# Performance work log

Hardware: AMD Instinct MI355X
Metric: run time of the kernel (lower is better)

Reference implementation:

```python
import jax, jax.numpy as jnp
import numpy as np

B = 16384       # batch
NCAT = 16       # number of categorical features / tokens
VOCAB = 1000    # per-feature vocab size
D = 64          # embedding_dim / d_model
H = 4           # num_heads
SHARED = 10     # max(1, int(64 * 1/6))
INDIV = D - SHARED  # 54
CONT = 16       # continuous feature dim
L = 2           # layers per encoder
FLAT = NCAT * D + CONT  # 1040, MLP input dim
EPS = 1e-5


def _ln(x, w, b):
    m = x.mean(-1, keepdims=True)
    v = ((x - m) ** 2).mean(-1, keepdims=True)
    return (x - m) / jnp.sqrt(v + EPS) * w + b


def _encoder(x, qkv_w, out_w, ln1w, ln1b, ln2w, ln2b, w1, b1, w2, b2):
    # x: [b, t, d]; stacked per-layer params have leading dim L, scanned over.
    b, t, d = x.shape
    dh = d // H
    scale = dh ** -0.5

    def step(carry, p):
        x, prev = carry
        qw, ow, l1w, l1b, l2w, l2b, fw1, fb1, fw2, fb2 = p
        xn = _ln(x, l1w, l1b)
        qkv = xn @ qw                       # [b, t, 3d]
        q, k, v = jnp.split(qkv, 3, axis=-1)
        q = q.reshape(b, t, H, dh).transpose(0, 2, 1, 3)  # [b, h, t, dh]
        k = k.reshape(b, t, H, dh).transpose(0, 2, 1, 3)
        v = v.reshape(b, t, H, dh).transpose(0, 2, 1, 3)
        scores = jnp.einsum('bhid,bhjd->bhij', q, k) * scale + prev
        attn = jax.nn.softmax(scores, axis=-1)
        o = jnp.einsum('bhij,bhjd->bhid', attn, v)
        o = o.transpose(0, 2, 1, 3).reshape(b, t, d) @ ow
        x = x + o
        ff = jax.nn.gelu(_ln(x, l2w, l2b) @ fw1 + fb1, approximate=False) @ fw2 + fb2
        # prev_attn is detached in the torch code
        return (x + ff, jax.lax.stop_gradient(scores)), None

    prev0 = jnp.zeros((b, H, t, t), x.dtype)
    (x, _), _ = jax.lax.scan(step, (x, prev0),
                             (qkv_w, out_w, ln1w, ln1b, ln2w, ln2b, w1, b1, w2, b2))
    return x


def setup_inputs() -> dict:
    key = jax.random.key(0)
    ks = iter(jax.random.split(key, 64))

    def rn(shape, s=0.02):
        return jax.random.normal(next(ks), shape, jnp.float32) * s

    inp = {}
    inp['x_cat'] = jax.random.randint(next(ks), (B, NCAT), 0, VOCAB)
    inp['x_cont'] = jax.random.normal(next(ks), (B, CONT), jnp.float32)
    inp['shared_emb'] = rn((SHARED,), 1.0)
    inp['emb_tables'] = rn((NCAT, VOCAB, INDIV), 1.0)
    for pfx in ('mi', 'ma'):
        inp[pfx + '_qkv'] = rn((L, D, 3 * D))
        inp[pfx + '_out'] = rn((L, D, D))
        inp[pfx + '_ln1w'] = jnp.ones((L, D)); inp[pfx + '_ln1b'] = jnp.zeros((L, D))
        inp[pfx + '_ln2w'] = jnp.ones((L, D)); inp[pfx + '_ln2b'] = jnp.zeros((L, D))
        inp[pfx + '_w1'] = rn((L, D, 4 * D)); inp[pfx + '_b1'] = jnp.zeros((L, 4 * D))
        inp[pfx + '_w2'] = rn((L, 4 * D, D)); inp[pfx + '_b2'] = jnp.zeros((L, D))
    inp['cont_w'] = rn((CONT, CONT)); inp['cont_b'] = jnp.zeros((CONT,))
    inp['mlp_w1'] = rn((FLAT, 4 * FLAT)); inp['mlp_b1'] = jnp.zeros((4 * FLAT,))
    inp['mlp_w2'] = rn((4 * FLAT, 2 * FLAT)); inp['mlp_b2'] = jnp.zeros((2 * FLAT,))
    inp['mlp_w3'] = rn((2 * FLAT, 1)); inp['mlp_b3'] = jnp.zeros((1,))
    return inp


def reference(x_cat, x_cont, shared_emb, emb_tables,
              mi_qkv, mi_out, mi_ln1w, mi_ln1b, mi_ln2w, mi_ln2b, mi_w1, mi_b1, mi_w2, mi_b2,
              ma_qkv, ma_out, ma_ln1w, ma_ln1b, ma_ln2w, ma_ln2b, ma_w1, ma_b1, ma_w2, ma_b2,
              cont_w, cont_b, mlp_w1, mlp_b1, mlp_w2, mlp_b2, mlp_w3, mlp_b3):
    b = x_cat.shape[0]
    # embed: shared prefix + per-feature individual embedding -> [b, NCAT, D]
    indiv = emb_tables[jnp.arange(NCAT)[None, :], x_cat]          # [b, NCAT, INDIV]
    shared = jnp.broadcast_to(shared_emb, (b, NCAT, SHARED))
    tokens = jnp.concatenate([shared, indiv], axis=-1)
    # micro encoder on tokens (0, 1)
    micro = _encoder(tokens[:, :2, :], mi_qkv, mi_out, mi_ln1w, mi_ln1b,
                     mi_ln2w, mi_ln2b, mi_w1, mi_b1, mi_w2, mi_b2)
    tokens = tokens.at[:, :2, :].set(micro)
    # macro encoder on all tokens
    macro = _encoder(tokens, ma_qkv, ma_out, ma_ln1w, ma_ln1b,
                     ma_ln2w, ma_ln2b, ma_w1, ma_b1, ma_w2, ma_b2)
    flat = macro.reshape(b, NCAT * D)
    cont = x_cont @ cont_w + cont_b
    x = jnp.concatenate([flat, cont], axis=-1)
    h = jax.nn.gelu(x @ mlp_w1 + mlp_b1, approximate=False)
    h = jax.nn.gelu(h @ mlp_w2 + mlp_b2, approximate=False)
    logits = (h @ mlp_w3 + mlp_b3)[:, 0]
    return logits
```

## Files before the change

### kernel.cpp

```cpp
#include <hip/hip_runtime.h>
#include <hip/hip_bf16.h>
#include <math.h>

#define BATCH  16384
#define NCATS  16
#define VOCABN 1000
#define DIMD   64
#define SHARED_E 10
#define INDIVE 54
#define CONTN  16
#define FLATN  1040
#define H1N    4160
#define H2N    2080
#define KP1    1088
#define NP1    4224
#define KP2    4224
#define NP2    2176
#define EPSV   1e-5f

typedef __attribute__((ext_vector_type(8))) short bf16x8;
typedef __attribute__((ext_vector_type(4))) float f32x4;

__device__ __forceinline__ float gelu_f(float x) {
    return 0.5f * x * (1.0f + erff(x * 0.70710678118654752440f));
}
__device__ __forceinline__ float wsum(float v) {
#pragma unroll
    for (int o = 32; o > 0; o >>= 1) v += __shfl_xor(v, o, 64);
    return v;
}
__device__ __forceinline__ short f2bf_s(float a) {
    __hip_bfloat16 x = __float2bfloat16(a);
    return *reinterpret_cast<short*>(&x);
}
__device__ __forceinline__ unsigned int packbf(float a, float b) {
    __hip_bfloat16 x = __float2bfloat16(a), y = __float2bfloat16(b);
    unsigned short ux = *reinterpret_cast<unsigned short*>(&x);
    unsigned short uy = *reinterpret_cast<unsigned short*>(&y);
    return (unsigned)ux | ((unsigned)uy << 16);
}
__device__ __forceinline__ float bf_lo(unsigned int u) { return __uint_as_float(u << 16); }
__device__ __forceinline__ float bf_hi(unsigned int u) { return __uint_as_float(u & 0xffff0000u); }
__device__ __forceinline__ void gload16(const void* g, void* l) {
    __builtin_amdgcn_global_load_lds(
        (const __attribute__((address_space(1))) void*)g,
        (__attribute__((address_space(3))) void*)l, 16, 0, 0);
}

__global__ __launch_bounds__(256) void build_tokens(
    const int* __restrict__ x_cat, const float* __restrict__ shared_emb,
    const float* __restrict__ emb, float* __restrict__ xflat)
{
    int idx = blockIdx.x * 256 + threadIdx.x;
    int b = idx >> 10, r = idx & 1023;
    int c = r >> 6, d = r & 63;
    float v;
    if (d < SHARED_E) v = shared_emb[d];
    else              v = emb[((size_t)c * VOCABN + x_cat[b * NCATS + c]) * INDIVE + (d - SHARED_E)];
    xflat[(size_t)b * FLATN + r] = v;
}

__global__ __launch_bounds__(256) void cont_proj(
    const float* __restrict__ x_cont, const float* __restrict__ cw,
    const float* __restrict__ cb, float* __restrict__ xflat)
{
    int idx = blockIdx.x * 256 + threadIdx.x;
    int b = idx >> 4, j = idx & 15;
    float acc = cb[j];
#pragma unroll
    for (int k = 0; k < 16; ++k) acc += x_cont[b * 16 + k] * cw[k * 16 + j];
    xflat[(size_t)b * FLATN + 1024 + j] = acc;
}

__global__ __launch_bounds__(64) void micro_enc_mfma(
    float* __restrict__ xflat, const short* __restrict__ wT,
    const float* __restrict__ ln1w, const float* __restrict__ ln1b,
    const float* __restrict__ ln2w, const float* __restrict__ ln2b,
    const float* __restrict__ b1, const float* __restrict__ b2)
{
    __shared__ __align__(16) float Xr[16][68];
    __shared__ __align__(16) short XN[16][72];
    __shared__ __align__(16) short KVb[16][136];
    __shared__ __align__(16) short Qb[16][72];

    int lane = threadIdx.x;
    int b0 = blockIdx.x * 8;

    {
        int r = lane >> 2, c0 = (lane & 3) * 16;
        const float* gx = xflat + (size_t)(b0 + (r >> 1)) * FLATN + (r & 1) * 64 + c0;
#pragma unroll
        for (int u = 0; u < 4; ++u) *(float4*)&Xr[r][c0 + u * 4] = *(const float4*)(gx + u * 4);
    }
    __syncthreads();

    int fr = lane & 15, fk = lane >> 4;
    int rb = 4 * fk;
    float prevM[2] = {0.f, 0.f};

    for (int p = 0; p < 2; ++p) {
        const short* lq  = wT + p * 49152;
        const short* lo  = lq + 12288;
        const short* lf1 = lo + 4096;
        const short* lf2 = lf1 + 16384;
        const float* l1w = ln1w + p * 64; const float* l1b = ln1b + p * 64;
        const float* l2w = ln2w + p * 64; const float* l2b = ln2b + p * 64;
        const float* fb1 = b1 + p * 256;  const float* fb2 = b2 + p * 64;

        {
            float wv = l1w[lane], bv = l1b[lane];
#pragma unroll
            for (int i = 0; i < 16; ++i) {
                float v = Xr[i][lane];
                float m = wsum(v) * (1.f / 64.f);
                float d = v - m;
                float var = wsum(d * d) * (1.f / 64.f);
                XN[i][lane] = f2bf_s(d * rsqrtf(var + EPSV) * wv + bv);
            }
        }
        __syncthreads();

        {
            bf16x8 a0 = *(const bf16x8*)&XN[fr][fk * 8];
            bf16x8 a1 = *(const bf16x8*)&XN[fr][fk * 8 + 32];
#pragma unroll
            for (int nf = 0; nf < 12; ++nf) {
                const short* bp = lq + (nf * 16 + fr) * 64 + fk * 8;
                bf16x8 bv0 = *(const bf16x8*)bp;
                bf16x8 bv1 = *(const bf16x8*)(bp + 32);
                f32x4 acc = {};
                acc = __builtin_amdgcn_mfma_f32_16x16x32_bf16(a0, bv0, acc, 0, 0, 0);
                acc = __builtin_amdgcn_mfma_f32_16x16x32_bf16(a1, bv1, acc, 0, 0, 0);
                int cc = nf * 16 + fr;
#pragma unroll
                for (int rr = 0; rr < 4; ++rr) {
                    if (nf < 4) Qb[rb + rr][cc] = f2bf_s(acc[rr]);
                    else        KVb[rb + rr][cc - 64] = f2bf_s(acc[rr]);
                }
            }
        }
        __syncthreads();

        {
            int s_ = lane >> 3, h = (lane >> 1) & 3, qi = lane & 1;
            int qrow = s_ * 2 + qi;
            float q[16];
            {
                const unsigned* qp = (const unsigned*)&Qb[qrow][h * 16];
#pragma unroll
                for (int e = 0; e < 8; ++e) { q[2 * e] = bf_lo(qp[e]); q[2 * e + 1] = bf_hi(qp[e]); }
            }
            float sc[2];
#pragma unroll
            for (int j = 0; j < 2; ++j) {
                const unsigned* kp = (const unsigned*)&KVb[s_ * 2 + j][h * 16];
                float a = 0.f;
#pragma unroll
                for (int e = 0; e < 8; ++e)
                    a += q[2 * e] * bf_lo(kp[e]) + q[2 * e + 1] * bf_hi(kp[e]);
                a = a * 0.25f + prevM[j];
                prevM[j] = a;
                sc[j] = a;
            }
            float mx = fmaxf(sc[0], sc[1]);
            float e0 = expf(sc[0] - mx), e1 = expf(sc[1] - mx);
            float inv = 1.f / (e0 + e1);
            float p0 = e0 * inv, p1 = e1 * inv;
            const unsigned* v0 = (const unsigned*)&KVb[s_ * 2 + 0][64 + h * 16];
            const unsigned* v1 = (const unsigned*)&KVb[s_ * 2 + 1][64 + h * 16];
            unsigned* op = (unsigned*)&XN[qrow][h * 16];
#pragma unroll
            for (int e = 0; e < 8; ++e) {
                unsigned ua = v0[e], ub = v1[e];
                float olo = p0 * bf_lo(ua) + p1 * bf_lo(ub);
                float ohi = p0 * bf_hi(ua) + p1 * bf_hi(ub);
                op[e] = packbf(olo, ohi);
            }
        }
        __syncthreads();

        {
            bf16x8 a0 = *(const bf16x8*)&XN[fr][fk * 8];
            bf16x8 a1 = *(const bf16x8*)&XN[fr][fk * 8 + 32];
#pragma unroll
            for (int nf = 0; nf < 4; ++nf) {
                const short* bp = lo + (nf * 16 + fr) * 64 + fk * 8;
                bf16x8 bv0 = *(const bf16x8*)bp;
                bf16x8 bv1 = *(const bf16x8*)(bp + 32);
                f32x4 acc = {};
                acc = __builtin_amdgcn_mfma_f32_16x16x32_bf16(a0, bv0, acc, 0, 0, 0);
                acc = __builtin_amdgcn_mfma_f32_16x16x32_bf16(a1, bv1, acc, 0, 0, 0);
                int cc = nf * 16 + fr;
#pragma unroll
                for (int rr = 0; rr < 4; ++rr) Xr[rb + rr][cc] += acc[rr];
            }
        }
        __syncthreads();

        {
            float wv = l2w[lane], bv = l2b[lane];
#pragma unroll
            for (int i = 0; i < 16; ++i) {
                float v = Xr[i][lane];
                float m = wsum(v) * (1.f / 64.f);
                float d = v - m;
                float var = wsum(d * d) * (1.f / 64.f);
                XN[i][lane] = f2bf_s(d * rsqrtf(var + EPSV) * wv + bv);
            }
        }
        __syncthreads();

        {
            bf16x8 a0 = *(const bf16x8*)&XN[fr][fk * 8];
            bf16x8 a1 = *(const bf16x8*)&XN[fr][fk * 8 + 32];
            f32x4 facc[4] = {};
#pragma unroll
            for (int half = 0; half < 2; ++half) {
#pragma unroll
                for (int nf = 0; nf < 8; ++nf) {
                    int ng = half * 128 + nf * 16;
                    const short* bp = lf1 + (ng + fr) * 64 + fk * 8;
                    bf16x8 bv0 = *(const bf16x8*)bp;
                    bf16x8 bv1 = *(const bf16x8*)(bp + 32);
                    f32x4 acc = {};
                    acc = __builtin_amdgcn_mfma_f32_16x16x32_bf16(a0, bv0, acc, 0, 0, 0);
                    acc = __builtin_amdgcn_mfma_f32_16x16x32_bf16(a1, bv1, acc, 0, 0, 0);
                    int cc = nf * 16 + fr;
                    float bias1 = fb1[ng + fr];
#pragma unroll
                    for (int rr = 0; rr < 4; ++rr)
                        KVb[rb + rr][cc] = f2bf_s(gelu_f(acc[rr] + bias1));
                }
                __syncthreads();
                bf16x8 fa[4];
#pragma unroll
                for (int kf = 0; kf < 4; ++kf)
                    fa[kf] = *(const bf16x8*)&KVb[fr][kf * 32 + fk * 8];
#pragma unroll
                for (int nf = 0; nf < 4; ++nf) {
                    const short* bp = lf2 + (nf * 16 + fr) * 256 + half * 128 + fk * 8;
#pragma unroll
                    for (int kf = 0; kf < 4; ++kf)
                        facc[nf] = __builtin_amdgcn_mfma_f32_16x16x32_bf16(
                            fa[kf], *(const bf16x8*)(bp + kf * 32), facc[nf], 0, 0, 0);
                }
                __syncthreads();
            }
#pragma unroll
            for (int nf = 0; nf < 4; ++nf) {
                int cc = nf * 16 + fr;
                float bias2 = fb2[cc];
#pragma unroll
                for (int rr = 0; rr < 4; ++rr) Xr[rb + rr][cc] += facc[nf][rr] + bias2;
            }
        }
        __syncthreads();
    }

    {
        int r = lane >> 2, c0 = (lane & 3) * 16;
        float* gx = xflat + (size_t)(b0 + (r >> 1)) * FLATN + (r & 1) * 64 + c0;
#pragma unroll
        for (int u = 0; u < 4; ++u) *(float4*)(gx + u * 4) = *(const float4*)&Xr[r][c0 + u * 4];
    }
}

__global__ __launch_bounds__(64) void macro_enc_mfma(
    float* __restrict__ xflat, __hip_bfloat16* __restrict__ Abf,
    const short* __restrict__ wT,
    const float* __restrict__ ln1w, const float* __restrict__ ln1b,
    const float* __restrict__ ln2w, const float* __restrict__ ln2b,
    const float* __restrict__ b1, const float* __restrict__ b2)
{
    __shared__ __align__(16) float Xr[16][68];
    __shared__ __align__(16) short XN[16][72];
    __shared__ __align__(16) short Qb[16][72];
    __shared__ __align__(16) short Kb[16][72];
    __shared__ __align__(16) short VT[16][72];

    int lane = threadIdx.x;
    int b = blockIdx.x;

    {
        int r = lane >> 2, c0 = (lane & 3) * 16;
        const float* gx = xflat + (size_t)b * FLATN + r * 64 + c0;
#pragma unroll
        for (int u = 0; u < 4; ++u) *(float4*)&Xr[r][c0 + u * 4] = *(const float4*)(gx + u * 4);
    }
    __syncthreads();

    int fr = lane & 15, fk = lane >> 4;
    int rb = 4 * fk;
    f32x4 prevA[4] = {};

    for (int p = 0; p < 2; ++p) {
        const short* lq  = wT + p * 49152;
        const short* lo  = lq + 12288;
        const short* lf1 = lo + 4096;
        const short* lf2 = lf1 + 16384;
        const float* l1w = ln1w + p * 64; const float* l1b = ln1b + p * 64;
        const float* l2w = ln2w + p * 64; const float* l2b = ln2b + p * 64;
        const float* fb1 = b1 + p * 256;  const float* fb2 = b2 + p * 64;

        {
            float wv = l1w[lane], bv = l1b[lane];
#pragma unroll
            for (int i = 0; i < 16; ++i) {
                float v = Xr[i][lane];
                float m = wsum(v) * (1.f / 64.f);
                float d = v - m;
                float var = wsum(d * d) * (1.f / 64.f);
                XN[i][lane] = f2bf_s(d * rsqrtf(var + EPSV) * wv + bv);
            }
        }
        __syncthreads();

        {
            bf16x8 a0 = *(const bf16x8*)&XN[fr][fk * 8];
            bf16x8 a1 = *(const bf16x8*)&XN[fr][fk * 8 + 32];
#pragma unroll
            for (int nf = 0; nf < 12; ++nf) {
                const short* bp = lq + (nf * 16 + fr) * 64 + fk * 8;
                bf16x8 bv0 = *(const bf16x8*)bp;
                bf16x8 bv1 = *(const bf16x8*)(bp + 32);
                f32x4 acc = {};
                acc = __builtin_amdgcn_mfma_f32_16x16x32_bf16(a0, bv0, acc, 0, 0, 0);
                acc = __builtin_amdgcn_mfma_f32_16x16x32_bf16(a1, bv1, acc, 0, 0, 0);
#pragma unroll
                for (int rr = 0; rr < 4; ++rr) {
                    short sv = f2bf_s(acc[rr]);
                    if (nf < 4)       Qb[rb + rr][nf * 16 + fr] = sv;
                    else if (nf < 8)  Kb[rb + rr][(nf - 4) * 16 + fr] = sv;
                    else              VT[fr][(nf - 8) * 16 + rb + rr] = sv;
                }
            }
        }
        __syncthreads();

        {
            bf16x8 zero8 = {};
#pragma unroll
            for (int h = 0; h < 4; ++h) {
                bf16x8 ka = zero8, qa = zero8, va = zero8;
                if (fk < 2) {
                    ka = *(const bf16x8*)&Kb[fr][h * 16 + fk * 8];
                    qa = *(const bf16x8*)&Qb[fr][h * 16 + fk * 8];
                    va = *(const bf16x8*)&VT[fr][h * 16 + fk * 8];
                }
                f32x4 s = {};
                s = __builtin_amdgcn_mfma_f32_16x16x32_bf16(ka, qa, s, 0, 0, 0);
#pragma unroll
                for (int rr = 0; rr < 4; ++rr) {
                    s[rr] = s[rr] * 0.25f + prevA[h][rr];
                    prevA[h][rr] = s[rr];
                }
                float m = fmaxf(fmaxf(s[0], s[1]), fmaxf(s[2], s[3]));
                m = fmaxf(m, __shfl_xor(m, 16, 64));
                m = fmaxf(m, __shfl_xor(m, 32, 64));
                float e0 = expf(s[0] - m), e1 = expf(s[1] - m);
                float e2 = expf(s[2] - m), e3 = expf(s[3] - m);
                float sum = e0 + e1 + e2 + e3;
                sum += __shfl_xor(sum, 16, 64);
                sum += __shfl_xor(sum, 32, 64);
                float inv = 1.f / sum;
                int pk0 = (int)packbf(e0 * inv, e1 * inv);
                int pk1 = (int)packbf(e2 * inv, e3 * inv);
                int s1 = fr + (((2 * fk) & 3) << 4);
                int s2 = fr + (((2 * fk + 1) & 3) << 4);
                int d0 = __shfl(pk0, s1, 64), d1 = __shfl(pk1, s1, 64);
                int d2 = __shfl(pk0, s2, 64), d3 = __shfl(pk1, s2, 64);
                bf16x8 pa = zero8;
                if (fk < 2) {
                    union { int i[4]; bf16x8 v; } u;
                    u.i[0] = d0; u.i[1] = d1; u.i[2] = d2; u.i[3] = d3;
                    pa = u.v;
                }
                f32x4 o = {};
                o = __builtin_amdgcn_mfma_f32_16x16x32_bf16(pa, va, o, 0, 0, 0);
#pragma unroll
                for (int rr = 0; rr < 4; ++rr)
                    XN[4 * fk + rr][h * 16 + fr] = f2bf_s(o[rr]);
            }
        }
        __syncthreads();

        {
            bf16x8 a0 = *(const bf16x8*)&XN[fr][fk * 8];
            bf16x8 a1 = *(const bf16x8*)&XN[fr][fk * 8 + 32];
#pragma unroll
            for (int nf = 0; nf < 4; ++nf) {
                const short* bp = lo + (nf * 16 + fr) * 64 + fk * 8;
                bf16x8 bv0 = *(const bf16x8*)bp;
                bf16x8 bv1 = *(const bf16x8*)(bp + 32);
                f32x4 acc = {};
                acc = __builtin_amdgcn_mfma_f32_16x16x32_bf16(a0, bv0, acc, 0, 0, 0);
                acc = __builtin_amdgcn_mfma_f32_16x16x32_bf16(a1, bv1, acc, 0, 0, 0);
                int cc = nf * 16 + fr;
#pragma unroll
                for (int rr = 0; rr < 4; ++rr) Xr[rb + rr][cc] += acc[rr];
            }
        }
        __syncthreads();

        {
            float wv = l2w[lane], bv = l2b[lane];
#pragma unroll
            for (int i = 0; i < 16; ++i) {
                float v = Xr[i][lane];
                float m = wsum(v) * (1.f / 64.f);
                float d = v - m;
                float var = wsum(d * d) * (1.f / 64.f);
                XN[i][lane] = f2bf_s(d * rsqrtf(var + EPSV) * wv + bv);
            }
        }
        __syncthreads();

        {
            bf16x8 a0 = *(const bf16x8*)&XN[fr][fk * 8];
            bf16x8 a1 = *(const bf16x8*)&XN[fr][fk * 8 + 32];
            f32x4 facc[4] = {};
#pragma unroll
            for (int half = 0; half < 2; ++half) {
#pragma unroll
                for (int nf = 0; nf < 8; ++nf) {
                    int ng = half * 128 + nf * 16;
                    const short* bp = lf1 + (ng + fr) * 64 + fk * 8;
                    bf16x8 bv0 = *(const bf16x8*)bp;
                    bf16x8 bv1 = *(const bf16x8*)(bp + 32);
                    f32x4 acc = {};
                    acc = __builtin_amdgcn_mfma_f32_16x16x32_bf16(a0, bv0, acc, 0, 0, 0);
                    acc = __builtin_amdgcn_mfma_f32_16x16x32_bf16(a1, bv1, acc, 0, 0, 0);
                    int cc = nf * 16 + fr;
                    float bias1 = fb1[ng + fr];
#pragma unroll
                    for (int rr = 0; rr < 4; ++rr) {
                        short sv = f2bf_s(gelu_f(acc[rr] + bias1));
                        if (cc < 64) Qb[rb + rr][cc] = sv;
                        else         Kb[rb + rr][cc - 64] = sv;
                    }
                }
                __syncthreads();
                bf16x8 fa[4];
                fa[0] = *(const bf16x8*)&Qb[fr][fk * 8];
                fa[1] = *(const bf16x8*)&Qb[fr][32 + fk * 8];
                fa[2] = *(const bf16x8*)&Kb[fr][fk * 8];
                fa[3] = *(const bf16x8*)&Kb[fr][32 + fk * 8];
#pragma unroll
                for (int nf = 0; nf < 4; ++nf) {
                    const short* bp = lf2 + (nf * 16 + fr) * 256 + half * 128 + fk * 8;
#pragma unroll
                    for (int kf = 0; kf < 4; ++kf)
                        facc[nf] = __builtin_amdgcn_mfma_f32_16x16x32_bf16(
                            fa[kf], *(const bf16x8*)(bp + kf * 32), facc[nf], 0, 0, 0);
                }
                __syncthreads();
            }
#pragma unroll
            for (int nf = 0; nf < 4; ++nf) {
                int cc = nf * 16 + fr;
                float bias2 = fb2[cc];
#pragma unroll
                for (int rr = 0; rr < 4; ++rr) Xr[rb + rr][cc] += facc[nf][rr] + bias2;
            }
        }
        __syncthreads();
    }

    {
        int r = lane >> 2, c0 = (lane & 3) * 16;
        float* gx = xflat + (size_t)b * FLATN + r * 64 + c0;
#pragma unroll
        for (int u = 0; u < 4; ++u) *(float4*)(gx + u * 4) = *(const float4*)&Xr[r][c0 + u * 4];
        unsigned int pk[8];
#pragma unroll
        for (int e = 0; e < 8; ++e) pk[e] = packbf(Xr[r][c0 + 2 * e], Xr[r][c0 + 2 * e + 1]);
        unsigned int* ga = (unsigned int*)(Abf + (size_t)b * KP1 + r * 64 + c0);
#pragma unroll
        for (int e = 0; e < 8; ++e) ga[e] = pk[e];
    }
    {
        float v = (lane < CONTN) ? xflat[(size_t)b * FLATN + 1024 + lane] : 0.f;
        Abf[(size_t)b * KP1 + 1024 + lane] = __float2bfloat16(v);
    }
}

__global__ __launch_bounds__(256) void transpose_conv(
    const float* __restrict__ src, __hip_bfloat16* __restrict__ dst,
    int K, int N, int Kp, int Np)
{
    __shared__ float T[32][33];
    int k0 = blockIdx.y * 32, n0 = blockIdx.x * 32;
    int tn = threadIdx.x & 31, tk = threadIdx.x >> 5;
#pragma unroll
    for (int r = 0; r < 4; ++r) {
        int k = k0 + tk + r * 8, n = n0 + tn;
        T[tk + r * 8][tn] = (k < K && n < N) ? src[(size_t)k * N + n] : 0.f;
    }
    __syncthreads();
#pragma unroll
    for (int r = 0; r < 4; ++r) {
        int n = n0 + tk + r * 8, k = k0 + tn;
        dst[(size_t)n * Kp + k] = __float2bfloat16(T[tn][tk + r * 8]);
    }
}

template <int MODE>
__global__ __launch_bounds__(256, 3) void gemm_mfma(
    const __hip_bfloat16* __restrict__ A, const __hip_bfloat16* __restrict__ Bt,
    const float* __restrict__ bias, int bias_n,
    __hip_bfloat16* __restrict__ Cbf, const float* __restrict__ w3,
    float* __restrict__ partials, int Np, int Kp)
{
    __shared__ __align__(16) short LDSbuf[16384];

    int tid = threadIdx.x;
    int lane = tid & 63, wave = tid >> 6;

    int nbx = gridDim.x;
    int nwg = nbx * gridDim.y;
    int wgid = blockIdx.y * nbx + blockIdx.x;
    int q = nwg >> 3, r = nwg & 7;
    int xcd = wgid & 7, loc = wgid >> 3;
    int sw = (xcd < r ? xcd * (q + 1) : r * (q + 1) + (xcd - r) * q) + loc;
    int bm = (sw / nbx) * 128, bx = sw % nbx, bn = bx * 128;

    int lrow8 = lane >> 3;
    int lk8sw = ((lane & 7) ^ lrow8) * 8;
    const __hip_bfloat16* Ag = A  + (size_t)(bm + wave * 32 + lrow8) * Kp + lk8sw;
    const __hip_bfloat16* Bg = Bt + (size_t)(bn + wave * 32 + lrow8) * Kp + lk8sw;
    short* Al = LDSbuf + wave * 32 * 64;
    short* Bl = Al + 8192;

    int wm = (wave >> 1) * 64, wn = (wave & 1) * 64;
    int lrow = lane & 15, lk = lane >> 4;
    int key = lane & 7;

    f32x4 acc[4][4] = {};
    int nt = Kp >> 6;

    for (int t = 0; t < nt; ++t) {
        int k0 = t << 6;
        __syncthreads();
#pragma unroll
        for (int it = 0; it < 4; ++it) {
            gload16(Ag + (size_t)(it * 8) * Kp + k0, Al + it * 8 * 64);
            gload16(Bg + (size_t)(it * 8) * Kp + k0, Bl + it * 8 * 64);
        }
        __syncthreads();
#pragma unroll
        for (int ks = 0; ks < 2; ++ks) {
            int so = ((ks * 4 + lk) ^ key) * 8;
            bf16x8 af[4], bf[4];
#pragma unroll
            for (int i = 0; i < 4; ++i) af[i] = *(const bf16x8*)(LDSbuf + (wm + i * 16 + lrow) * 64 + so);
#pragma unroll
            for (int j = 0; j < 4; ++j) bf[j] = *(const bf16x8*)(LDSbuf + 8192 + (wn + j * 16 + lrow) * 64 + so);
#pragma unroll
            for (int i = 0; i < 4; ++i)
#pragma unroll
                for (int j = 0; j < 4; ++j)
                    acc[i][j] = __builtin_amdgcn_mfma_f32_16x16x32_bf16(af[i], bf[j], acc[i][j], 0, 0, 0);
        }
    }
    __syncthreads();

    if (MODE == 1) {
        short* Cs = LDSbuf;
#pragma unroll
        for (int j = 0; j < 4; ++j) {
            int cl = wn + j * 16 + lrow;
            float bv = (bn + cl < bias_n) ? bias[bn + cl] : 0.f;
#pragma unroll
            for (int i = 0; i < 4; ++i) {
#pragma unroll
                for (int rr = 0; rr < 4; ++rr) {
                    int rl = wm + i * 16 + 4 * lk + rr;
                    int pos = ((((cl >> 3) ^ (rl & 7)) << 3) | (cl & 7));
                    Cs[rl * 128 + pos] = f2bf_s(gelu_f(acc[i][j][rr] + bv));
                }
            }
        }
        __syncthreads();
        int rloc = tid >> 1, half = tid & 1;
        int4* dst = (int4*)(Cbf + (size_t)(bm + rloc) * Np + bn + half * 64);
#pragma unroll
        for (int u = 0; u < 8; ++u) {
            int slot = half * 8 + (u ^ (rloc & 7));
            dst[u] = *(const int4*)&Cs[rloc * 128 + slot * 8];
        }
    } else {
        float rs[16];
#pragma unroll
        for (int t = 0; t < 16; ++t) rs[t] = 0.f;
#pragma unroll
        for (int j = 0; j < 4; ++j) {
            int gcol = bn + wn + j * 16 + lrow;
            float bv  = (gcol < bias_n) ? bias[gcol] : 0.f;
            float w3v = (gcol < H2N) ? w3[gcol] : 0.f;
#pragma unroll
            for (int i = 0; i < 4; ++i)
#pragma unroll
                for (int rr = 0; rr < 4; ++rr)
                    rs[i * 4 + rr] += gelu_f(acc[i][j][rr] + bv) * w3v;
        }
#pragma unroll
        for (int o = 1; o < 16; o <<= 1)
#pragma unroll
            for (int t = 0; t < 16; ++t) rs[t] += __shfl_xor(rs[t], o, 64);
        float* pr = (float*)LDSbuf;
        if (lrow == 0) {
#pragma unroll
            for (int i = 0; i < 4; ++i)
#pragma unroll
                for (int rr = 0; rr < 4; ++rr)
                    pr[(wm + i * 16 + 4 * lk + rr) * 2 + (wave & 1)] = rs[i * 4 + rr];
        }
        __syncthreads();
        if (tid < 128)
            partials[(size_t)(bm + tid) * nbx + bx] = pr[tid * 2] + pr[tid * 2 + 1];
    }
}

__global__ __launch_bounds__(256) void reduce_partials(
    const float* __restrict__ partials, const float* __restrict__ b3,
    float* __restrict__ out, int n, int nbx)
{
    int b = blockIdx.x * 256 + threadIdx.x;
    if (b >= n) return;
    float s = b3[0];
    for (int x = 0; x < nbx; ++x) s += partials[(size_t)b * nbx + x];
    out[b] = s;
}

extern "C" void kernel_launch(void* const* d_in, const int* in_sizes, int n_in,
                              void* d_out, int out_size, void* d_ws, size_t ws_size,
                              hipStream_t stream)
{
    const int*   x_cat      = (const int*)  d_in[0];
    const float* x_cont     = (const float*)d_in[1];
    const float* shared_emb = (const float*)d_in[2];
    const float* emb        = (const float*)d_in[3];
    const float* mi_qkv  = (const float*)d_in[4];
    const float* mi_out  = (const float*)d_in[5];
    const float* mi_ln1w = (const float*)d_in[6];
    const float* mi_ln1b = (const float*)d_in[7];
    const float* mi_ln2w = (const float*)d_in[8];
    const float* mi_ln2b = (const float*)d_in[9];
    const float* mi_w1   = (const float*)d_in[10];
    const float* mi_b1   = (const float*)d_in[11];
    const float* mi_w2   = (const float*)d_in[12];
    const float* mi_b2   = (const float*)d_in[13];
    const float* ma_qkv  = (const float*)d_in[14];
    const float* ma_out  = (const float*)d_in[15];
    const float* ma_ln1w = (const float*)d_in[16];
    const float* ma_ln1b = (const float*)d_in[17];
    const float* ma_ln2w = (const float*)d_in[18];
    const float* ma_ln2b = (const float*)d_in[19];
    const float* ma_w1   = (const float*)d_in[20];
    const float* ma_b1   = (const float*)d_in[21];
    const float* ma_w2   = (const float*)d_in[22];
    const float* ma_b2   = (const float*)d_in[23];
    const float* cont_w  = (const float*)d_in[24];
    const float* cont_b  = (const float*)d_in[25];
    const float* w1      = (const float*)d_in[26];
    const float* b1      = (const float*)d_in[27];
    const float* w2      = (const float*)d_in[28];
    const float* b2      = (const float*)d_in[29];
    const float* w3      = (const float*)d_in[30];
    const float* b3      = (const float*)d_in[31];
    float* out = (float*)d_out;

    const int NBX2 = NP2 / 128;
    const size_t ENC_SH = 4 * 49152;
    const size_t FIXED = ((size_t)NP1 * KP1 + (size_t)NP2 * KP2 + ENC_SH) * 2;
    const size_t PER_ROW = (size_t)NP1 * 2 + (size_t)FLATN * 4 + (size_t)KP1 * 2 + (size_t)NBX2 * 4;
    size_t avail = (ws_size > FIXED) ? ws_size - FIXED : 0;
    long long chl = (long long)(avail / PER_ROW);
    int CH = (int)((chl / 128) * 128);
    if (CH > BATCH) CH = BATCH;
    if (CH < 128) CH = 128;

    char* p = (char*)d_ws;
    __hip_bfloat16* w1T = (__hip_bfloat16*)p; p += (size_t)NP1 * KP1 * 2;
    __hip_bfloat16* w2T = (__hip_bfloat16*)p; p += (size_t)NP2 * KP2 * 2;
    __hip_bfloat16* encT = (__hip_bfloat16*)p; p += ENC_SH * 2;
    __hip_bfloat16* h1  = (__hip_bfloat16*)p; p += (size_t)CH * NP1 * 2;
    float* xflat = (float*)p;                 p += (size_t)CH * FLATN * 4;
    __hip_bfloat16* Abf = (__hip_bfloat16*)p; p += (size_t)CH * KP1 * 2;
    float* partials = (float*)p;

    transpose_conv<<<dim3(NP1 / 32, KP1 / 32), 256, 0, stream>>>(w1, w1T, FLATN, H1N, KP1, NP1);
    transpose_conv<<<dim3(NP2 / 32, KP2 / 32), 256, 0, stream>>>(w2, w2T, H1N, H2N, KP2, NP2);

    const float* enc_qkv[2] = {ma_qkv, mi_qkv};
    const float* enc_out[2] = {ma_out, mi_out};
    const float* enc_w1[2]  = {ma_w1,  mi_w1};
    const float* enc_w2[2]  = {ma_w2,  mi_w2};
    for (int grp = 0; grp < 2; ++grp) {
        for (int pl = 0; pl < 2; ++pl) {
            __hip_bfloat16* base = encT + (size_t)(grp * 2 + pl) * 49152;
            transpose_conv<<<dim3(192 / 32, 64 / 32), 256, 0, stream>>>(
                enc_qkv[grp] + pl * 64 * 192, base, 64, 192, 64, 192);
            transpose_conv<<<dim3(64 / 32, 64 / 32), 256, 0, stream>>>(
                enc_out[grp] + pl * 64 * 64, base + 12288, 64, 64, 64, 64);
            transpose_conv<<<dim3(256 / 32, 64 / 32), 256, 0, stream>>>(
                enc_w1[grp] + pl * 64 * 256, base + 16384, 64, 256, 64, 256);
            transpose_conv<<<dim3(64 / 32, 256 / 32), 256, 0, stream>>>(
                enc_w2[grp] + pl * 256 * 64, base + 32768, 256, 64, 256, 64);
        }
    }

    for (int m0 = 0; m0 < BATCH; m0 += CH) {
        int mc = BATCH - m0 < CH ? BATCH - m0 : CH;

        build_tokens<<<(mc * 1024) / 256, 256, 0, stream>>>(
            x_cat + (size_t)m0 * NCATS, shared_emb, emb, xflat);
        cont_proj<<<(mc * 16) / 256, 256, 0, stream>>>(
            x_cont + (size_t)m0 * CONTN, cont_w, cont_b, xflat);
        micro_enc_mfma<<<mc / 8, 64, 0, stream>>>(
            xflat, (const short*)encT + 2 * 49152, mi_ln1w, mi_ln1b, mi_ln2w, mi_ln2b, mi_b1, mi_b2);
        macro_enc_mfma<<<mc, 64, 0, stream>>>(
            xflat, Abf, (const short*)encT, ma_ln1w, ma_ln1b, ma_ln2w, ma_ln2b, ma_b1, ma_b2);

        gemm_mfma<1><<<dim3(NP1 / 128, mc / 128), 256, 0, stream>>>(
            Abf, w1T, b1, H1N, h1, nullptr, nullptr, NP1, KP1);
        gemm_mfma<2><<<dim3(NBX2, mc / 128), 256, 0, stream>>>(
            h1, w2T, b2, H2N, nullptr, w3, partials, NP2, KP2);

        reduce_partials<<<(mc + 255) / 256, 256, 0, stream>>>(partials, b3, out + m0, mc, NBX2);
    }
}
```

Baseline: 1.369 ms.

## Split macro encoder work across two wavefronts per sample block

The macro encoder kernel now launches 128 threads (two wavefronts) per sample instead of one. LayerNorm rows, QKV output tiles, attention heads, output projection columns and FFN tiles are divided between the two waves, and each wave keeps only its own prevA and facc state. This shortens the serial per-block critical path and lowers register pressure per wave. In exchange, the existing __syncthreads barriers now coordinate two waves, and the FFN staging through shared Qb/Kb must stay consistent when both waves write it.

After: 1.293 ms. 5.6% less time.

```diff
diff --git a/kernel.cpp b/kernel.cpp
--- a/kernel.cpp
+++ b/kernel.cpp
@@ -265,7 +265,7 @@
     }
 }
 
-__global__ __launch_bounds__(64) void macro_enc_mfma(
+__global__ __launch_bounds__(128) void macro_enc_mfma(
     float* __restrict__ xflat, __hip_bfloat16* __restrict__ Abf,
     const short* __restrict__ wT,
     const float* __restrict__ ln1w, const float* __restrict__ ln1b,
@@ -278,20 +278,21 @@
     __shared__ __align__(16) short Kb[16][72];
     __shared__ __align__(16) short VT[16][72];
 
-    int lane = threadIdx.x;
+    int tid = threadIdx.x;
+    int lane = tid & 63, w = tid >> 6;
     int b = blockIdx.x;
 
     {
-        int r = lane >> 2, c0 = (lane & 3) * 16;
+        int r = tid >> 3, c0 = (tid & 7) * 8;
         const float* gx = xflat + (size_t)b * FLATN + r * 64 + c0;
-#pragma unroll
-        for (int u = 0; u < 4; ++u) *(float4*)&Xr[r][c0 + u * 4] = *(const float4*)(gx + u * 4);
+        *(float4*)&Xr[r][c0]     = *(const float4*)gx;
+        *(float4*)&Xr[r][c0 + 4] = *(const float4*)(gx + 4);
     }
     __syncthreads();
 
     int fr = lane & 15, fk = lane >> 4;
     int rb = 4 * fk;
-    f32x4 prevA[4] = {};
+    f32x4 prevA[2] = {};
 
     for (int p = 0; p < 2; ++p) {
         const short* lq  = wT + p * 49152;
@@ -305,7 +306,8 @@
         {
             float wv = l1w[lane], bv = l1b[lane];
 #pragma unroll
-            for (int i = 0; i < 16; ++i) {
+            for (int i2 = 0; i2 < 8; ++i2) {
+                int i = w * 8 + i2;
                 float v = Xr[i][lane];
                 float m = wsum(v) * (1.f / 64.f);
                 float d = v - m;
@@ -319,7 +321,8 @@
             bf16x8 a0 = *(const bf16x8*)&XN[fr][fk * 8];
             bf16x8 a1 = *(const bf16x8*)&XN[fr][fk * 8 + 32];
 #pragma unroll
-            for (int nf = 0; nf < 12; ++nf) {
+            for (int nn = 0; nn < 6; ++nn) {
+                int nf = w * 6 + nn;
                 const short* bp = lq + (nf * 16 + fr) * 64 + fk * 8;
                 bf16x8 bv0 = *(const bf16x8*)bp;
                 bf16x8 bv1 = *(const bf16x8*)(bp + 32);
@@ -340,7 +343,8 @@
         {
             bf16x8 zero8 = {};
 #pragma unroll
-            for (int h = 0; h < 4; ++h) {
+            for (int hh = 0; hh < 2; ++hh) {
+                int h = 2 * w + hh;
                 bf16x8 ka = zero8, qa = zero8, va = zero8;
                 if (fk < 2) {
                     ka = *(const bf16x8*)&Kb[fr][h * 16 + fk * 8];
@@ -351,8 +355,8 @@
                 s = __builtin_amdgcn_mfma_f32_16x16x32_bf16(ka, qa, s, 0, 0, 0);
 #pragma unroll
                 for (int rr = 0; rr < 4; ++rr) {
-                    s[rr] = s[rr] * 0.25f + prevA[h][rr];
-                    prevA[h][rr] = s[rr];
+                    s[rr] = s[rr] * 0.25f + prevA[hh][rr];
+                    prevA[hh][rr] = s[rr];
                 }
                 float m = fmaxf(fmaxf(s[0], s[1]), fmaxf(s[2], s[3]));
                 m = fmaxf(m, __shfl_xor(m, 16, 64));
@@ -388,7 +392,8 @@
             bf16x8 a0 = *(const bf16x8*)&XN[fr][fk * 8];
             bf16x8 a1 = *(const bf16x8*)&XN[fr][fk * 8 + 32];
 #pragma unroll
-            for (int nf = 0; nf < 4; ++nf) {
+            for (int nn = 0; nn < 2; ++nn) {
+                int nf = w * 2 + nn;
                 const short* bp = lo + (nf * 16 + fr) * 64 + fk * 8;
                 bf16x8 bv0 = *(const bf16x8*)bp;
                 bf16x8 bv1 = *(const bf16x8*)(bp + 32);
@@ -405,7 +410,8 @@
         {
             float wv = l2w[lane], bv = l2b[lane];
 #pragma unroll
-            for (int i = 0; i < 16; ++i) {
+            for (int i2 = 0; i2 < 8; ++i2) {
+                int i = w * 8 + i2;
                 float v = Xr[i][lane];
                 float m = wsum(v) * (1.f / 64.f);
                 float d = v - m;
@@ -418,11 +424,12 @@
         {
             bf16x8 a0 = *(const bf16x8*)&XN[fr][fk * 8];
             bf16x8 a1 = *(const bf16x8*)&XN[fr][fk * 8 + 32];
-            f32x4 facc[4] = {};
+            f32x4 facc[2] = {};
 #pragma unroll
             for (int half = 0; half < 2; ++half) {
 #pragma unroll
-                for (int nf = 0; nf < 8; ++nf) {
+                for (int nn = 0; nn < 4; ++nn) {
+                    int nf = w * 4 + nn;
                     int ng = half * 128 + nf * 16;
                     const short* bp = lf1 + (ng + fr) * 64 + fk * 8;
                     bf16x8 bv0 = *(const bf16x8*)bp;
@@ -446,41 +453,42 @@
                 fa[2] = *(const bf16x8*)&Kb[fr][fk * 8];
                 fa[3] = *(const bf16x8*)&Kb[fr][32 + fk * 8];
 #pragma unroll
-                for (int nf = 0; nf < 4; ++nf) {
+                for (int nn = 0; nn < 2; ++nn) {
+                    int nf = w * 2 + nn;
                     const short* bp = lf2 + (nf * 16 + fr) * 256 + half * 128 + fk * 8;
 #pragma unroll
                     for (int kf = 0; kf < 4; ++kf)
-                        facc[nf] = __builtin_amdgcn_mfma_f32_16x16x32_bf16(
-                            fa[kf], *(const bf16x8*)(bp + kf * 32), facc[nf], 0, 0, 0);
+                        facc[nn] = __builtin_amdgcn_mfma_f32_16x16x32_bf16(
+                            fa[kf], *(const bf16x8*)(bp + kf * 32), facc[nn], 0, 0, 0);
                 }
                 __syncthreads();
             }
 #pragma unroll
-            for (int nf = 0; nf < 4; ++nf) {
-                int cc = nf * 16 + fr;
+            for (int nn = 0; nn < 2; ++nn) {
+                int cc = (w * 2 + nn) * 16 + fr;
                 float bias2 = fb2[cc];
 #pragma unroll
-                for (int rr = 0; rr < 4; ++rr) Xr[rb + rr][cc] += facc[nf][rr] + bias2;
+                for (int rr = 0; rr < 4; ++rr) Xr[rb + rr][cc] += facc[nn][rr] + bias2;
             }
         }
         __syncthreads();
     }
 
     {
-        int r = lane >> 2, c0 = (lane & 3) * 16;
+        int r = tid >> 3, c0 = (tid & 7) * 8;
         float* gx = xflat + (size_t)b * FLATN + r * 64 + c0;
-#pragma unroll
-        for (int u = 0; u < 4; ++u) *(float4*)(gx + u * 4) = *(const float4*)&Xr[r][c0 + u * 4];
-        unsigned int pk[8];
-#pragma unroll
-        for (int e = 0; e < 8; ++e) pk[e] = packbf(Xr[r][c0 + 2 * e], Xr[r][c0 + 2 * e + 1]);
+        *(float4*)gx       = *(const float4*)&Xr[r][c0];
+        *(float4*)(gx + 4) = *(const float4*)&Xr[r][c0 + 4];
+        unsigned int pk[4];
+#pragma unroll
+        for (int e = 0; e < 4; ++e) pk[e] = packbf(Xr[r][c0 + 2 * e], Xr[r][c0 + 2 * e + 1]);
         unsigned int* ga = (unsigned int*)(Abf + (size_t)b * KP1 + r * 64 + c0);
 #pragma unroll
-        for (int e = 0; e < 8; ++e) ga[e] = pk[e];
-    }
-    {
-        float v = (lane < CONTN) ? xflat[(size_t)b * FLATN + 1024 + lane] : 0.f;
-        Abf[(size_t)b * KP1 + 1024 + lane] = __float2bfloat16(v);
+        for (int e = 0; e < 4; ++e) ga[e] = pk[e];
+    }
+    if (tid < 64) {
+        float v = (tid < CONTN) ? xflat[(size_t)b * FLATN + 1024 + tid] : 0.f;
+        Abf[(size_t)b * KP1 + 1024 + tid] = __float2bfloat16(v);
     }
 }
 
@@ -719,7 +727,7 @@
             x_cont + (size_t)m0 * CONTN, cont_w, cont_b, xflat);
         micro_enc_mfma<<<mc / 8, 64, 0, stream>>>(
             xflat, (const short*)encT + 2 * 49152, mi_ln1w, mi_ln1b, mi_ln2w, mi_ln2b, mi_b1, mi_b2);
-        macro_enc_mfma<<<mc, 64, 0, stream>>>(
+        macro_enc_mfma<<<mc, 128, 0, stream>>>(
             xflat, Abf, (const short*)encT, ma_ln1w, ma_ln1b, ma_ln2w, ma_ln2b, ma_b1, ma_b2);
 
         gemm_mfma<1><<<dim3(NP1 / 128, mc / 128), 256, 0, stream>>>(
```
